# Kernel tuning notes

Hardware: AMD Instinct MI355X
Metric: run time of the kernel (lower is better)

Reference implementation:

```python
import jax, jax.numpy as jnp
import numpy as np

LEAKY_SLOPE = 0.2
ALPHA, BETA = 1.0, 0.1
CLAMP_MAX = 40.0

N_NODES, N_FEAT = 20000, 128
N_EDGES, N_QUERY = 320000, 200000
B = 512            # boundary matrix size
DIM = 8            # 'dimension' hyperparam


def setup_inputs() -> dict:
    key = jax.random.key(0)
    ks = jax.random.split(key, 20)
    sc = 1.0 / np.sqrt(B)
    inp = {
        'x': jax.random.normal(ks[0], (N_NODES, N_FEAT), jnp.float32),
        'L0': jax.random.normal(ks[1], (B, B), jnp.float32) * sc,
        'L1': jax.random.normal(ks[2], (B, B), jnp.float32) * sc,
        'edge_index': jax.random.randint(ks[3], (2, N_EDGES), 0, N_NODES),
        'total_edges': jax.random.randint(ks[4], (N_QUERY, 2), 0, N_NODES),
        # learned params (Linear weights stored as [in, out])
        'conv1_W': jax.random.normal(ks[5], (N_FEAT, 64), jnp.float32) * 0.05,
        'conv1_b': jnp.zeros((64,), jnp.float32),
        'conv2_W': jax.random.normal(ks[6], (64, 32), jnp.float32) * 0.05,
        'conv2_b': jnp.zeros((32,), jnp.float32),
        'weights_sim': jax.random.normal(ks[7], (2 * B, DIM), jnp.float32) * 0.05,
        'embeddings_sim': jax.random.normal(ks[8], (N_FEAT, 2 * B), jnp.float32) * 0.05,
        'weights_off_diagonal': jax.random.normal(ks[9], (B, B), jnp.float32) * sc,
        'weights_L_0': jax.random.normal(ks[10], (B, 32), jnp.float32) * 0.05,
        'weights_L_1': jax.random.normal(ks[11], (B, 32), jnp.float32) * 0.05,
        'lin1_W': jax.random.normal(ks[12], (DIM + 32, 32), jnp.float32) * 0.1,
        'lin1_b': jnp.zeros((32,), jnp.float32),
        'lin_W': jax.random.normal(ks[13], (32, 1), jnp.float32) * 0.1,
        'lin_b': jnp.zeros((1,), jnp.float32),
    }
    return inp


def _renorm_rows(v):
    # torch renorm_(2, 0, 1): rescale rows whose L2 norm exceeds 1
    n = jnp.linalg.norm(v, axis=1, keepdims=True)
    return v * jnp.where(n > 1.0, 1.0 / (n + 1e-7), 1.0)


def _gcn_conv(h, src, dst, dinv, W, b):
    h = h @ W
    msg = h[src] * (dinv[src] * dinv[dst])[:, None]
    return jax.ops.segment_sum(msg, dst, num_segments=h.shape[0]) + b


def reference(x, L0, L1, edge_index, total_edges,
              conv1_W, conv1_b, conv2_W, conv2_b,
              weights_sim, embeddings_sim, weights_off_diagonal,
              weights_L_0, weights_L_1, lin1_W, lin1_b, lin_W, lin_b):
    N = x.shape[0]
    # --- g_encode: two GCN layers (eval mode, dropout = identity) ---
    loops = jnp.arange(N)
    src = jnp.concatenate([edge_index[0], loops])
    dst = jnp.concatenate([edge_index[1], loops])
    deg = jax.ops.segment_sum(jnp.ones_like(dst, dtype=x.dtype), dst, num_segments=N)
    dinv = jnp.where(deg > 0, jax.lax.rsqrt(jnp.maximum(deg, 1.0)), 0.0)
    h = jax.nn.relu(_gcn_conv(x, src, dst, dinv, conv1_W, conv1_b))
    g_emb = jax.nn.relu(_gcn_conv(h, src, dst, dinv, conv2_W, conv2_b))  # [N, 32]

    # --- s_encode: boundary-matrix block + softmax ---
    L0_r = L0 @ L0
    L1_r = L1 @ L1
    rel = (L0_r @ weights_L_0) @ (L1_r @ weights_L_1).T          # [B, B]
    rel_ = weights_off_diagonal @ rel                             # [B, B]
    upper = jnp.concatenate([L0_r, rel_], axis=1)
    lower = jnp.concatenate([rel_.T, L1_r], axis=1)
    sim_block = jax.nn.softmax(jax.nn.relu(jnp.concatenate([upper, lower], axis=0)), axis=1)  # [2B, 2B]

    s_emb = ((x @ embeddings_sim) @ sim_block) @ weights_sim      # [N, DIM]
    s_emb = _renorm_rows(s_emb)
    g = _renorm_rows(g_emb)

    # --- edge gather + distance MLP ---
    i0, i1 = total_edges[:, 0], total_edges[:, 1]
    d_sim = jnp.square(s_emb[i0] - s_emb[i1])                     # [Eq, DIM]
    g_sq = jnp.square(g[i0] - g[i1])                              # [Eq, 32]
    feat = jnp.concatenate([ALPHA * g_sq, BETA * d_sim], axis=1)  # [Eq, 40]
    hq = jax.nn.leaky_relu(feat @ lin1_W + lin1_b, LEAKY_SLOPE)
    sqdist = jnp.abs(hq @ lin_W + lin_b).reshape(-1)
    sqdist = jnp.clip(sqdist, 0.0, CLAMP_MAX)
    prob = jax.nn.sigmoid(2.0 - sqdist)  # == 1/(exp(sqdist-2)+1)
    return prob
```

## Files before the change

### kernel.cpp

```cpp
#include <hip/hip_runtime.h>
#include <math.h>

#define NE 320000
#define NN 20000
#define NQ 200000


__device__ __forceinline__ void gemm512_body(char* smem, const float* __restrict__ A,
                                             float* __restrict__ C, int bb) {
  float (*As)[68] = (float(*)[68])smem;
  float (*Bs)[68] = (float(*)[68])(smem + 16 * 68 * 4);
  int tid = threadIdx.x;
  int tx = tid & 15, ty = tid >> 4;
  int brow = (bb >> 3) * 64;
  int bcol = (bb & 7) * 64;
  float c[4][4] = {};
  for (int k0 = 0; k0 < 512; k0 += 16) {
#pragma unroll
    for (int t = 0; t < 4; t++) {
      int idx = tid * 4 + t;
      int r = idx >> 4, cc = idx & 15;
      As[cc][r] = A[(size_t)(brow + r) * 512 + k0 + cc];
      int r2 = idx >> 6, c2 = idx & 63;
      Bs[r2][c2] = A[(size_t)(k0 + r2) * 512 + bcol + c2];
    }
    __syncthreads();
#pragma unroll
    for (int k = 0; k < 16; k++) {
      float a0 = As[k][ty * 4 + 0], a1 = As[k][ty * 4 + 1];
      float a2 = As[k][ty * 4 + 2], a3 = As[k][ty * 4 + 3];
      float b0 = Bs[k][tx * 4 + 0], b1 = Bs[k][tx * 4 + 1];
      float b2 = Bs[k][tx * 4 + 2], b3 = Bs[k][tx * 4 + 3];
      c[0][0] = fmaf(a0, b0, c[0][0]); c[0][1] = fmaf(a0, b1, c[0][1]);
      c[0][2] = fmaf(a0, b2, c[0][2]); c[0][3] = fmaf(a0, b3, c[0][3]);
      c[1][0] = fmaf(a1, b0, c[1][0]); c[1][1] = fmaf(a1, b1, c[1][1]);
      c[1][2] = fmaf(a1, b2, c[1][2]); c[1][3] = fmaf(a1, b3, c[1][3]);
      c[2][0] = fmaf(a2, b0, c[2][0]); c[2][1] = fmaf(a2, b1, c[2][1]);
      c[2][2] = fmaf(a2, b2, c[2][2]); c[2][3] = fmaf(a2, b3, c[2][3]);
      c[3][0] = fmaf(a3, b0, c[3][0]); c[3][1] = fmaf(a3, b1, c[3][1]);
      c[3][2] = fmaf(a3, b2, c[3][2]); c[3][3] = fmaf(a3, b3, c[3][3]);
    }
    __syncthreads();
  }
#pragma unroll
  for (int i = 0; i < 4; i++)
#pragma unroll
    for (int j = 0; j < 4; j++)
      C[(size_t)(brow + ty * 4 + i) * 512 + bcol + tx * 4 + j] = c[i][j];
}

template<int K, int N>
__device__ __forceinline__ void xw_body(char* smem, const float* __restrict__ X,
                                        const float* __restrict__ W,
                                        float* __restrict__ Y, int bb) {
  constexpr int TPR = N / 4;
  constexpr int ROWS = 256 / TPR;
  float* Wl = (float*)smem;
  for (int t = threadIdx.x; t < K * N / 4; t += 256)
    ((float4*)Wl)[t] = ((const float4*)W)[t];
  __syncthreads();
  int r = bb * ROWS + threadIdx.x / TPR;
  int c4 = (threadIdx.x % TPR) * 4;
  if (r >= NN) return;
  const float4* xr4 = (const float4*)(X + (size_t)r * K);
  float a0 = 0, a1 = 0, a2 = 0, a3 = 0;
#pragma unroll 4
  for (int k4 = 0; k4 < K / 4; k4++) {
    float4 xv = xr4[k4];
    int kb = k4 * 4;
    { const float4 w = *(const float4*)&Wl[(kb + 0) * N + c4];
      a0 = fmaf(xv.x, w.x, a0); a1 = fmaf(xv.x, w.y, a1); a2 = fmaf(xv.x, w.z, a2); a3 = fmaf(xv.x, w.w, a3); }
    { const float4 w = *(const float4*)&Wl[(kb + 1) * N + c4];
      a0 = fmaf(xv.y, w.x, a0); a1 = fmaf(xv.y, w.y, a1); a2 = fmaf(xv.y, w.z, a2); a3 = fmaf(xv.y, w.w, a3); }
    { const float4 w = *(const float4*)&Wl[(kb + 2) * N + c4];
      a0 = fmaf(xv.z, w.x, a0); a1 = fmaf(xv.z, w.y, a1); a2 = fmaf(xv.z, w.z, a2); a3 = fmaf(xv.z, w.w, a3); }
    { const float4 w = *(const float4*)&Wl[(kb + 3) * N + c4];
      a0 = fmaf(xv.w, w.x, a0); a1 = fmaf(xv.w, w.y, a1); a2 = fmaf(xv.w, w.z, a2); a3 = fmaf(xv.w, w.w, a3); }
  }
  float4 o; o.x = a0; o.y = a1; o.z = a2; o.w = a3;
  *(float4*)&Y[(size_t)r * N + c4] = o;
}

__device__ __forceinline__ void sk512_body(const float* X, const float* W, float* Y, int b) {
  int r = b * 32 + threadIdx.x / 8;
  int c4 = (threadIdx.x % 8) * 4;
  const float4* xr4 = (const float4*)(X + (size_t)r * 512);
  float a0 = 0, a1 = 0, a2 = 0, a3 = 0;
#pragma unroll 2
  for (int k4 = 0; k4 < 128; k4++) {
    float4 xv = xr4[k4];
    int kb = k4 * 4;
    { const float4 w = *(const float4*)&W[(kb + 0) * 32 + c4];
      a0 = fmaf(xv.x, w.x, a0); a1 = fmaf(xv.x, w.y, a1); a2 = fmaf(xv.x, w.z, a2); a3 = fmaf(xv.x, w.w, a3); }
    { const float4 w = *(const float4*)&W[(kb + 1) * 32 + c4];
      a0 = fmaf(xv.y, w.x, a0); a1 = fmaf(xv.y, w.y, a1); a2 = fmaf(xv.y, w.z, a2); a3 = fmaf(xv.y, w.w, a3); }
    { const float4 w = *(const float4*)&W[(kb + 2) * 32 + c4];
      a0 = fmaf(xv.z, w.x, a0); a1 = fmaf(xv.z, w.y, a1); a2 = fmaf(xv.z, w.z, a2); a3 = fmaf(xv.z, w.w, a3); }
    { const float4 w = *(const float4*)&W[(kb + 3) * 32 + c4];
      a0 = fmaf(xv.w, w.x, a0); a1 = fmaf(xv.w, w.y, a1); a2 = fmaf(xv.w, w.z, a2); a3 = fmaf(xv.w, w.w, a3); }
  }
  float4 o; o.x = a0; o.y = a1; o.z = a2; o.w = a3;
  *(float4*)&Y[(size_t)r * 32 + c4] = o;
}


__global__ __launch_bounds__(256) void mega1(const float* __restrict__ L0,
                                             const float* __restrict__ L1,
                                             float* __restrict__ L0r,
                                             float* __restrict__ L1r,
                                             const float* __restrict__ x,
                                             const float* __restrict__ W1,
                                             float* __restrict__ h1raw,
                                             int* __restrict__ ideg) {
  __shared__ __align__(16) char smem[32768];
  int b = blockIdx.x;
  if (b < 128) {
    const float* A = (b < 64) ? L0 : L1;
    float* C = (b < 64) ? L0r : L1r;
    gemm512_body(smem, A, C, b & 63);
  } else if (b < 1378) {
    xw_body<128, 64>(smem, x, W1, h1raw, b - 128);
  } else {
    int i = (b - 1378) * 256 + threadIdx.x;
    if (i < NN) ideg[i] = 0;
  }
}

__global__ __launch_bounds__(256) void mega2(const float* __restrict__ L0r,
                                             const float* __restrict__ L1r,
                                             const float* __restrict__ wL0,
                                             const float* __restrict__ wL1,
                                             float* __restrict__ Ab,
                                             float* __restrict__ Bb,
                                             const int* __restrict__ ei,
                                             int* __restrict__ ideg) {
  int b = blockIdx.x;
  if (b < 16) sk512_body(L0r, wL0, Ab, b);
  else if (b < 32) sk512_body(L1r, wL1, Bb, b - 16);
  else {
    int e = (b - 32) * 256 + threadIdx.x;
    if (e < NE) atomicAdd(&ideg[ei[NE + e]], 1);
  }
}

__global__ __launch_bounds__(256) void mega3(const float* __restrict__ wod,
                                             const float* __restrict__ Ab,
                                             float* __restrict__ Ab2,
                                             const int* __restrict__ ideg,
                                             int* __restrict__ start,
                                             int* __restrict__ cursor,
                                             float* __restrict__ dinv) {
  int b = blockIdx.x;
  if (b < 16) { sk512_body(wod, Ab, Ab2, b); return; }
  __shared__ int wsum[4];
  int t = threadIdx.x;
  int base = t * 80;
  int4 c[20];
  const int4* ip = (const int4*)ideg + t * 20;
#pragma unroll
  for (int i = 0; i < 20; i++) c[i] = ip[i];
  int s = 0;
  if (base < NN) {
#pragma unroll
    for (int i = 0; i < 20; i++) s += c[i].x + c[i].y + c[i].z + c[i].w;
  }
  int lane = t & 63, wid = t >> 6;
  int v = s;
#pragma unroll
  for (int o = 1; o < 64; o <<= 1) { int u = __shfl_up(v, o); if (lane >= o) v += u; }
  if (lane == 63) wsum[wid] = v;
  __syncthreads();
  int wbase = 0;
  for (int w = 0; w < wid; w++) wbase += wsum[w];
  int off = wbase + v - s;
  if (base < NN) {
#pragma unroll
    for (int i = 0; i < 20; i++) {
      int4 cc = c[i];
      int4 st;
      st.x = off; off += cc.x;
      st.y = off; off += cc.y;
      st.z = off; off += cc.z;
      st.w = off; off += cc.w;
      ((int4*)start)[t * 20 + i] = st;
      ((int4*)cursor)[t * 20 + i] = st;
      float4 dv;
      dv.x = rsqrtf((float)(cc.x + 1));
      dv.y = rsqrtf((float)(cc.y + 1));
      dv.z = rsqrtf((float)(cc.z + 1));
      dv.w = rsqrtf((float)(cc.w + 1));
      ((float4*)dinv)[t * 20 + i] = dv;
    }
  }
}

__global__ __launch_bounds__(256) void mega4(const float* __restrict__ L0r,
                                             const float* __restrict__ L1r,
                                             const float* __restrict__ Ab2,
                                             const float* __restrict__ Bb,
                                             const float* __restrict__ wsim,
                                             float* __restrict__ M,
                                             const int* __restrict__ ei,
                                             int* __restrict__ cursor,
                                             int* __restrict__ csr) {
  int b = blockIdx.x;
  if (b >= 1024) {
    int e = (b - 1024) * 256 + threadIdx.x;
    if (e < NE) {
      int d = ei[NE + e];
      int pos = atomicAdd(&cursor[d], 1);
      csr[pos] = ei[e];
    }
    return;
  }
  int i = b;
  int tid = threadIdx.x;
  float urow[32];
  {
    const float4* up = (const float4*)((i < 512) ? (Ab2 + i * 32) : (Bb + (i - 512) * 32));
#pragma unroll
    for (int q = 0; q < 8; q++) {
      float4 u4 = up[q];
      urow[q * 4 + 0] = u4.x; urow[q * 4 + 1] = u4.y;
      urow[q * 4 + 2] = u4.z; urow[q * 4 + 3] = u4.w;
    }
  }
  float loc[4];
  float mymax = 0.0f;
#pragma unroll
  for (int t = 0; t < 4; t++) {
    int j = tid + t * 256;
    float v;
    if (i < 512) {
      if (j < 512) v = L0r[i * 512 + j];
      else {
        const float4* bj = (const float4*)(Bb + (j - 512) * 32);
        float acc = 0.0f;
#pragma unroll
        for (int q = 0; q < 8; q++) {
          float4 b4 = bj[q];
          acc = fmaf(urow[q * 4 + 0], b4.x, acc); acc = fmaf(urow[q * 4 + 1], b4.y, acc);
          acc = fmaf(urow[q * 4 + 2], b4.z, acc); acc = fmaf(urow[q * 4 + 3], b4.w, acc);
        }
        v = acc;
      }
    } else {
      int r = i - 512;
      if (j < 512) {
        const float4* aj = (const float4*)(Ab2 + j * 32);
        float acc = 0.0f;
#pragma unroll
        for (int q = 0; q < 8; q++) {
          float4 a4 = aj[q];
          acc = fmaf(urow[q * 4 + 0], a4.x, acc); acc = fmaf(urow[q * 4 + 1], a4.y, acc);
          acc = fmaf(urow[q * 4 + 2], a4.z, acc); acc = fmaf(urow[q * 4 + 3], a4.w, acc);
        }
        v = acc;
      } else v = L1r[r * 512 + (j - 512)];
    }
    v = fmaxf(v, 0.0f);
    loc[t] = v;
    mymax = fmaxf(mymax, v);
  }
#pragma unroll
  for (int o = 32; o > 0; o >>= 1) mymax = fmaxf(mymax, __shfl_down(mymax, o));
  __shared__ float smax[4];
  int wid = tid >> 6, lane = tid & 63;
  if (lane == 0) smax[wid] = mymax;
  __syncthreads();
  float m = fmaxf(fmaxf(smax[0], smax[1]), fmaxf(smax[2], smax[3]));

  float z = 0.0f, pm[8] = {};
#pragma unroll
  for (int t = 0; t < 4; t++) {
    int j = tid + t * 256;
    float e = __expf(loc[t] - m);
    z += e;
    const float* wr = wsim + j * 8;
#pragma unroll
    for (int d = 0; d < 8; d++) pm[d] = fmaf(e, wr[d], pm[d]);
  }
#pragma unroll
  for (int o = 32; o > 0; o >>= 1) {
    z += __shfl_down(z, o);
#pragma unroll
    for (int d = 0; d < 8; d++) pm[d] += __shfl_down(pm[d], o);
  }
  __shared__ float sred[4][9];
  if (lane == 0) {
    sred[wid][0] = z;
#pragma unroll
    for (int d = 0; d < 8; d++) sred[wid][1 + d] = pm[d];
  }
  __syncthreads();
  if (tid < 8) {
    float zt = sred[0][0] + sred[1][0] + sred[2][0] + sred[3][0];
    float pt = sred[0][1 + tid] + sred[1][1 + tid] + sred[2][1 + tid] + sred[3][1 + tid];
    M[i * 8 + tid] = pt / zt;
  }
}

__global__ __launch_bounds__(256) void mega5(const int* __restrict__ start,
                                             const int* __restrict__ ideg,
                                             const int* __restrict__ csr,
                                             const float* __restrict__ hraw,
                                             const float* __restrict__ dinv,
                                             const float* __restrict__ b1,
                                             float* __restrict__ hout,
                                             const float* __restrict__ emb,
                                             const float* __restrict__ M,
                                             float* __restrict__ E) {
  int b = blockIdx.x;
  if (b < 5000) {
    int lane = threadIdx.x & 63;
    int n = b * 4 + (threadIdx.x >> 6);
    int s0 = start[n], cnt = ideg[n];
    float acc = 0.0f;
    int k = 0;
    for (; k + 1 < cnt; k += 2) {
      int sA = csr[s0 + k], sB = csr[s0 + k + 1];
      float dA = dinv[sA], dB = dinv[sB];
      float vA = hraw[(size_t)sA * 64 + lane];
      float vB = hraw[(size_t)sB * 64 + lane];
      acc = fmaf(vA, dA, acc);
      acc = fmaf(vB, dB, acc);
    }
    if (k < cnt) {
      int sA = csr[s0 + k];
      acc = fmaf(hraw[(size_t)sA * 64 + lane], dinv[sA], acc);
    }
    float dn = dinv[n];
    float v = fmaf(acc, dn, hraw[(size_t)n * 64 + lane] * dn * dn) + b1[lane];
    hout[(size_t)n * 64 + lane] = fmaxf(v, 0.0f);
    return;
  }
  int lane = threadIdx.x & 63;
  int r = (b - 5000) * 4 + (threadIdx.x >> 6);
  const float* er = emb + (size_t)r * 1024;
  float acc[8] = {};
  for (int it = 0; it < 16; it++) {
    int k = lane + it * 64;
    float e = er[k];
    const float4* mp = (const float4*)&M[k * 8];
    float4 m0 = mp[0], m1 = mp[1];
    acc[0] = fmaf(e, m0.x, acc[0]); acc[1] = fmaf(e, m0.y, acc[1]);
    acc[2] = fmaf(e, m0.z, acc[2]); acc[3] = fmaf(e, m0.w, acc[3]);
    acc[4] = fmaf(e, m1.x, acc[4]); acc[5] = fmaf(e, m1.y, acc[5]);
    acc[6] = fmaf(e, m1.z, acc[6]); acc[7] = fmaf(e, m1.w, acc[7]);
  }
#pragma unroll
  for (int o = 32; o > 0; o >>= 1)
#pragma unroll
    for (int d = 0; d < 8; d++) acc[d] += __shfl_down(acc[d], o);
  if (lane == 0)
#pragma unroll
    for (int d = 0; d < 8; d++) E[r * 8 + d] = acc[d];
}

__global__ __launch_bounds__(256) void mega6(const float* __restrict__ h1,
                                             const float* __restrict__ W2,
                                             float* __restrict__ h2raw,
                                             const float* __restrict__ x,
                                             const float* __restrict__ E,
                                             float* __restrict__ semb) {
  __shared__ __align__(16) char smem[8192];
  int b = blockIdx.x;
  if (b < 625) { xw_body<64, 32>(smem, h1, W2, h2raw, b); return; }
  float* El = (float*)smem;
  for (int t = threadIdx.x; t < 256; t += 256)
    ((float4*)El)[t] = ((const float4*)E)[t];
  __syncthreads();
  int row = (b - 625) * 256 + threadIdx.x;
  if (row >= NN) return;
  const float4* xr4 = (const float4*)(x + (size_t)row * 128);
  float s[8] = {};
#pragma unroll 4
  for (int k4 = 0; k4 < 32; k4++) {
    float4 xv = xr4[k4];
    int kb = k4 * 4;
#pragma unroll
    for (int u = 0; u < 4; u++) {
      float xk = (u == 0) ? xv.x : (u == 1) ? xv.y : (u == 2) ? xv.z : xv.w;
      const float4* ep = (const float4*)&El[(kb + u) * 8];
      float4 e0 = ep[0], e1 = ep[1];
      s[0] = fmaf(xk, e0.x, s[0]); s[1] = fmaf(xk, e0.y, s[1]);
      s[2] = fmaf(xk, e0.z, s[2]); s[3] = fmaf(xk, e0.w, s[3]);
      s[4] = fmaf(xk, e1.x, s[4]); s[5] = fmaf(xk, e1.y, s[5]);
      s[6] = fmaf(xk, e1.z, s[6]); s[7] = fmaf(xk, e1.w, s[7]);
    }
  }
  float n2 = 0.0f;
#pragma unroll
  for (int d = 0; d < 8; d++) n2 += s[d] * s[d];
  float n = sqrtf(n2);
  float sc = (n > 1.0f) ? 1.0f / (n + 1e-7f) : 1.0f;
#pragma unroll
  for (int d = 0; d < 8; d++) semb[(size_t)row * 8 + d] = s[d] * sc;
}

__global__ __launch_bounds__(256) void mega7(const int* __restrict__ start,
                                             const int* __restrict__ ideg,
                                             const int* __restrict__ csr,
                                             const float* __restrict__ hraw,
                                             const float* __restrict__ dinv,
                                             const float* __restrict__ b2,
                                             float* __restrict__ g) {
  int lane = threadIdx.x & 31;
  int n = blockIdx.x * 8 + (threadIdx.x >> 5);
  int s0 = start[n], cnt = ideg[n];
  float acc = 0.0f;
  int k = 0;
  for (; k + 1 < cnt; k += 2) {
    int sA = csr[s0 + k], sB = csr[s0 + k + 1];
    float dA = dinv[sA], dB = dinv[sB];
    float vA = hraw[(size_t)sA * 32 + lane];
    float vB = hraw[(size_t)sB * 32 + lane];
    acc = fmaf(vA, dA, acc);
    acc = fmaf(vB, dB, acc);
  }
  if (k < cnt) {
    int sA = csr[s0 + k];
    acc = fmaf(hraw[(size_t)sA * 32 + lane], dinv[sA], acc);
  }
  float dn = dinv[n];
  float v = fmaf(acc, dn, hraw[(size_t)n * 32 + lane] * dn * dn) + b2[lane];
  v = fmaxf(v, 0.0f);
  float n2 = v * v;
#pragma unroll
  for (int o = 16; o > 0; o >>= 1) n2 += __shfl_xor(n2, o);
  float nrm = sqrtf(n2);
  float sc = (nrm > 1.0f) ? 1.0f / (nrm + 1e-7f) : 1.0f;
  g[(size_t)n * 32 + lane] = v * sc;
}

__global__ __launch_bounds__(256) void mega8(const int* __restrict__ te,
                                             const float* __restrict__ g,
                                             const float* __restrict__ semb,
                                             const float* __restrict__ W1,
                                             const float* __restrict__ b1,
                                             const float* __restrict__ lw,
                                             const float* __restrict__ lb,
                                             float* __restrict__ out) {
  int q = blockIdx.x * 256 + threadIdx.x;
  if (q >= NQ) return;
  const int2 p = ((const int2*)te)[q];
  int i0 = p.x, i1 = p.y;
  float feat[40];
  const float4* g0 = (const float4*)(g + (size_t)i0 * 32);
  const float4* g1 = (const float4*)(g + (size_t)i1 * 32);
#pragma unroll
  for (int t = 0; t < 8; t++) {
    float4 a = g0[t], b = g1[t];
    float d0 = a.x - b.x, d1 = a.y - b.y, d2 = a.z - b.z, d3 = a.w - b.w;
    feat[t * 4 + 0] = d0 * d0; feat[t * 4 + 1] = d1 * d1;
    feat[t * 4 + 2] = d2 * d2; feat[t * 4 + 3] = d3 * d3;
  }
  const float4* s0 = (const float4*)(semb + (size_t)i0 * 8);
  const float4* s1 = (const float4*)(semb + (size_t)i1 * 8);
#pragma unroll
  for (int t = 0; t < 2; t++) {
    float4 a = s0[t], b = s1[t];
    float d0 = a.x - b.x, d1 = a.y - b.y, d2 = a.z - b.z, d3 = a.w - b.w;
    feat[32 + t * 4 + 0] = 0.1f * d0 * d0; feat[32 + t * 4 + 1] = 0.1f * d1 * d1;
    feat[32 + t * 4 + 2] = 0.1f * d2 * d2; feat[32 + t * 4 + 3] = 0.1f * d3 * d3;
  }
  float acc[32];
#pragma unroll
  for (int c = 0; c < 32; c++) acc[c] = b1[c];
#pragma unroll
  for (int k = 0; k < 40; k++) {
    float f = feat[k];
#pragma unroll
    for (int c = 0; c < 32; c++) acc[c] = fmaf(f, W1[k * 32 + c], acc[c]);
  }
  float accv = lb[0];
#pragma unroll
  for (int c = 0; c < 32; c++) {
    float a = acc[c];
    a = (a > 0.0f) ? a : 0.2f * a;
    accv = fmaf(a, lw[c], accv);
  }
  float sq = fminf(fabsf(accv), 40.0f);
  out[q] = 1.0f / (1.0f + __expf(sq - 2.0f));
}

extern "C" void kernel_launch(void* const* d_in, const int* in_sizes, int n_in,
                              void* d_out, int out_size, void* d_ws, size_t ws_size,
                              hipStream_t stream) {
  const float* x     = (const float*)d_in[0];
  const float* L0    = (const float*)d_in[1];
  const float* L1    = (const float*)d_in[2];
  const int*   ei    = (const int*)d_in[3];
  const int*   te    = (const int*)d_in[4];
  const float* W1    = (const float*)d_in[5];
  const float* b1    = (const float*)d_in[6];
  const float* W2    = (const float*)d_in[7];
  const float* b2    = (const float*)d_in[8];
  const float* wsim  = (const float*)d_in[9];
  const float* embs  = (const float*)d_in[10];
  const float* wod   = (const float*)d_in[11];
  const float* wL0   = (const float*)d_in[12];
  const float* wL1   = (const float*)d_in[13];
  const float* lin1W = (const float*)d_in[14];
  const float* lin1b = (const float*)d_in[15];
  const float* linW  = (const float*)d_in[16];
  const float* linb  = (const float*)d_in[17];
  float* out = (float*)d_out;

  int*   ideg   = (int*)d_ws;
  int*   start  = ideg + 20000;
  int*   cursor = start + 20000;
  int*   csr    = cursor + 20000;
  float* dinv   = (float*)(csr + 320000);
  float* h1raw  = dinv + 20000;
  float* h1     = h1raw + 1280000;
  float* h2raw  = h1raw;
  float* g      = h1 + 1280000;
  float* L0r    = g + 640000;
  float* L1r    = L0r + 262144;
  float* Ab     = L1r + 262144;
  float* Bb     = Ab + 16384;
  float* Ab2    = Bb + 16384;
  float* Mm     = Ab2 + 16384;
  float* Ee     = Mm + 8192;
  float* semb   = Ee + 1024;

  mega1<<<1457, 256, 0, stream>>>(L0, L1, L0r, L1r, x, W1, h1raw, ideg);
  mega2<<<1282, 256, 0, stream>>>(L0r, L1r, wL0, wL1, Ab, Bb, ei, ideg);
  mega3<<<17,   256, 0, stream>>>(wod, Ab, Ab2, ideg, start, cursor, dinv);
  mega4<<<2274, 256, 0, stream>>>(L0r, L1r, Ab2, Bb, wsim, Mm, ei, cursor, csr);
  mega5<<<5032, 256, 0, stream>>>(start, ideg, csr, h1raw, dinv, b1, h1, embs, Mm, Ee);
  mega6<<<704,  256, 0, stream>>>(h1, W2, h2raw, x, Ee, semb);
  mega7<<<2500, 256, 0, stream>>>(start, ideg, csr, h2raw, dinv, b2, g);
  mega8<<<782,  256, 0, stream>>>(te, g, semb, lin1W, lin1b, linW, linb, out);
}
```

Measured before the change: 186.4 us.

## Fuse eight phase kernels into one persistent cooperative kernel with grid syncs

Replaces the eight separate kernel launches with a single cooperative persistent kernel. Its blocks loop over each phase's tiles, with grid.sync between phases, so per-launch overhead and inter-kernel gaps go away. Shared memory is capped at 16KB so more blocks fit per CU, which means xw_body now stages the weight matrix in K-chunks. The final MLP is split into two 16-column halves to cut register pressure. Separate launches remain as a fallback if the cooperative launch fails. The trade-off is grid-wide barrier cost, and small phases (such as the 17-block scan) leaving most blocks idle.

Measured after the change: 668.7 us. +258.7%, slower.

```diff
diff --git a/kernel.cpp b/kernel.cpp
--- a/kernel.cpp
+++ b/kernel.cpp
@@ -1,10 +1,21 @@
 #include <hip/hip_runtime.h>
+#include <hip/hip_cooperative_groups.h>
 #include <math.h>
+
+namespace cg = cooperative_groups;
 
 #define NE 320000
 #define NN 20000
 #define NQ 200000
 
+struct Prm {
+  const float *x, *L0, *L1;
+  const int *ei, *te;
+  const float *W1, *b1, *W2, *b2, *wsim, *embs, *wod, *wL0, *wL1, *lin1W, *lin1b, *linW, *linb;
+  float *out;
+  int *ideg, *start, *cursor, *csr;
+  float *dinv, *h1raw, *h1, *g, *L0r, *L1r, *Ab, *Bb, *Ab2, *Mm, *Ee, *semb;
+};
 
 __device__ __forceinline__ void gemm512_body(char* smem, const float* __restrict__ A,
                                              float* __restrict__ C, int bb) {
@@ -55,30 +66,38 @@
                                         float* __restrict__ Y, int bb) {
   constexpr int TPR = N / 4;
   constexpr int ROWS = 256 / TPR;
+  constexpr int KC = (K * N * 4 > 16384) ? (16384 / (N * 4)) : K;
   float* Wl = (float*)smem;
-  for (int t = threadIdx.x; t < K * N / 4; t += 256)
-    ((float4*)Wl)[t] = ((const float4*)W)[t];
-  __syncthreads();
   int r = bb * ROWS + threadIdx.x / TPR;
   int c4 = (threadIdx.x % TPR) * 4;
-  if (r >= NN) return;
-  const float4* xr4 = (const float4*)(X + (size_t)r * K);
   float a0 = 0, a1 = 0, a2 = 0, a3 = 0;
+#pragma unroll 1
+  for (int k0 = 0; k0 < K; k0 += KC) {
+    for (int t = threadIdx.x; t < KC * N / 4; t += 256)
+      ((float4*)Wl)[t] = ((const float4*)(W + k0 * N))[t];
+    __syncthreads();
+    if (r < NN) {
+      const float4* xr4 = (const float4*)(X + (size_t)r * K + k0);
 #pragma unroll 4
-  for (int k4 = 0; k4 < K / 4; k4++) {
-    float4 xv = xr4[k4];
-    int kb = k4 * 4;
-    { const float4 w = *(const float4*)&Wl[(kb + 0) * N + c4];
-      a0 = fmaf(xv.x, w.x, a0); a1 = fmaf(xv.x, w.y, a1); a2 = fmaf(xv.x, w.z, a2); a3 = fmaf(xv.x, w.w, a3); }
-    { const float4 w = *(const float4*)&Wl[(kb + 1) * N + c4];
-      a0 = fmaf(xv.y, w.x, a0); a1 = fmaf(xv.y, w.y, a1); a2 = fmaf(xv.y, w.z, a2); a3 = fmaf(xv.y, w.w, a3); }
-    { const float4 w = *(const float4*)&Wl[(kb + 2) * N + c4];
-      a0 = fmaf(xv.z, w.x, a0); a1 = fmaf(xv.z, w.y, a1); a2 = fmaf(xv.z, w.z, a2); a3 = fmaf(xv.z, w.w, a3); }
-    { const float4 w = *(const float4*)&Wl[(kb + 3) * N + c4];
-      a0 = fmaf(xv.w, w.x, a0); a1 = fmaf(xv.w, w.y, a1); a2 = fmaf(xv.w, w.z, a2); a3 = fmaf(xv.w, w.w, a3); }
-  }
-  float4 o; o.x = a0; o.y = a1; o.z = a2; o.w = a3;
-  *(float4*)&Y[(size_t)r * N + c4] = o;
+      for (int k4 = 0; k4 < KC / 4; k4++) {
+        float4 xv = xr4[k4];
+        int kb = k4 * 4;
+        { const float4 w = *(const float4*)&Wl[(kb + 0) * N + c4];
+          a0 = fmaf(xv.x, w.x, a0); a1 = fmaf(xv.x, w.y, a1); a2 = fmaf(xv.x, w.z, a2); a3 = fmaf(xv.x, w.w, a3); }
+        { const float4 w = *(const float4*)&Wl[(kb + 1) * N + c4];
+          a0 = fmaf(xv.y, w.x, a0); a1 = fmaf(xv.y, w.y, a1); a2 = fmaf(xv.y, w.z, a2); a3 = fmaf(xv.y, w.w, a3); }
+        { const float4 w = *(const float4*)&Wl[(kb + 2) * N + c4];
+          a0 = fmaf(xv.z, w.x, a0); a1 = fmaf(xv.z, w.y, a1); a2 = fmaf(xv.z, w.z, a2); a3 = fmaf(xv.z, w.w, a3); }
+        { const float4 w = *(const float4*)&Wl[(kb + 3) * N + c4];
+          a0 = fmaf(xv.w, w.x, a0); a1 = fmaf(xv.w, w.y, a1); a2 = fmaf(xv.w, w.z, a2); a3 = fmaf(xv.w, w.w, a3); }
+      }
+    }
+    __syncthreads();
+  }
+  if (r < NN) {
+    float4 o; o.x = a0; o.y = a1; o.z = a2; o.w = a3;
+    *(float4*)&Y[(size_t)r * N + c4] = o;
+  }
 }
 
 __device__ __forceinline__ void sk512_body(const float* X, const float* W, float* Y, int b) {
@@ -104,67 +123,41 @@
 }
 
 
-__global__ __launch_bounds__(256) void mega1(const float* __restrict__ L0,
-                                             const float* __restrict__ L1,
-                                             float* __restrict__ L0r,
-                                             float* __restrict__ L1r,
-                                             const float* __restrict__ x,
-                                             const float* __restrict__ W1,
-                                             float* __restrict__ h1raw,
-                                             int* __restrict__ ideg) {
-  __shared__ __align__(16) char smem[32768];
-  int b = blockIdx.x;
-  if (b < 128) {
-    const float* A = (b < 64) ? L0 : L1;
-    float* C = (b < 64) ? L0r : L1r;
-    gemm512_body(smem, A, C, b & 63);
-  } else if (b < 1378) {
-    xw_body<128, 64>(smem, x, W1, h1raw, b - 128);
+__device__ __forceinline__ void phase0(const Prm& p, char* smem, int t) {
+  if (t < 128) {
+    gemm512_body(smem, (t < 64) ? p.L0 : p.L1, (t < 64) ? p.L0r : p.L1r, t & 63);
+  } else if (t < 1378) {
+    xw_body<128, 64>(smem, p.x, p.W1, p.h1raw, t - 128);
   } else {
-    int i = (b - 1378) * 256 + threadIdx.x;
-    if (i < NN) ideg[i] = 0;
-  }
-}
-
-__global__ __launch_bounds__(256) void mega2(const float* __restrict__ L0r,
-                                             const float* __restrict__ L1r,
-                                             const float* __restrict__ wL0,
-                                             const float* __restrict__ wL1,
-                                             float* __restrict__ Ab,
-                                             float* __restrict__ Bb,
-                                             const int* __restrict__ ei,
-                                             int* __restrict__ ideg) {
-  int b = blockIdx.x;
-  if (b < 16) sk512_body(L0r, wL0, Ab, b);
-  else if (b < 32) sk512_body(L1r, wL1, Bb, b - 16);
+    int i = (t - 1378) * 256 + threadIdx.x;
+    if (i < NN) p.ideg[i] = 0;
+  }
+}
+
+__device__ __forceinline__ void phase1(const Prm& p, int t) {
+  if (t < 16) sk512_body(p.L0r, p.wL0, p.Ab, t);
+  else if (t < 32) sk512_body(p.L1r, p.wL1, p.Bb, t - 16);
   else {
-    int e = (b - 32) * 256 + threadIdx.x;
-    if (e < NE) atomicAdd(&ideg[ei[NE + e]], 1);
-  }
-}
-
-__global__ __launch_bounds__(256) void mega3(const float* __restrict__ wod,
-                                             const float* __restrict__ Ab,
-                                             float* __restrict__ Ab2,
-                                             const int* __restrict__ ideg,
-                                             int* __restrict__ start,
-                                             int* __restrict__ cursor,
-                                             float* __restrict__ dinv) {
-  int b = blockIdx.x;
-  if (b < 16) { sk512_body(wod, Ab, Ab2, b); return; }
-  __shared__ int wsum[4];
-  int t = threadIdx.x;
-  int base = t * 80;
+    int e = (t - 32) * 256 + threadIdx.x;
+    if (e < NE) atomicAdd(&p.ideg[p.ei[NE + e]], 1);
+  }
+}
+
+__device__ __forceinline__ void phase2(const Prm& p, char* smem, int t) {
+  int tid = threadIdx.x;
+  if (t < 16) { sk512_body(p.wod, p.Ab, p.Ab2, t); return; }
+  int* wsum = (int*)smem;
+  int base = tid * 80;
   int4 c[20];
-  const int4* ip = (const int4*)ideg + t * 20;
-#pragma unroll
-  for (int i = 0; i < 20; i++) c[i] = ip[i];
   int s = 0;
   if (base < NN) {
+    const int4* ip = (const int4*)p.ideg + tid * 20;
+#pragma unroll
+    for (int i = 0; i < 20; i++) c[i] = ip[i];
 #pragma unroll
     for (int i = 0; i < 20; i++) s += c[i].x + c[i].y + c[i].z + c[i].w;
   }
-  int lane = t & 63, wid = t >> 6;
+  int lane = tid & 63, wid = tid >> 6;
   int v = s;
 #pragma unroll
   for (int o = 1; o < 64; o <<= 1) { int u = __shfl_up(v, o); if (lane >= o) v += u; }
@@ -182,42 +175,36 @@
       st.y = off; off += cc.y;
       st.z = off; off += cc.z;
       st.w = off; off += cc.w;
-      ((int4*)start)[t * 20 + i] = st;
-      ((int4*)cursor)[t * 20 + i] = st;
+      ((int4*)p.start)[tid * 20 + i] = st;
+      ((int4*)p.cursor)[tid * 20 + i] = st;
       float4 dv;
       dv.x = rsqrtf((float)(cc.x + 1));
       dv.y = rsqrtf((float)(cc.y + 1));
       dv.z = rsqrtf((float)(cc.z + 1));
       dv.w = rsqrtf((float)(cc.w + 1));
-      ((float4*)dinv)[t * 20 + i] = dv;
-    }
-  }
-}
-
-__global__ __launch_bounds__(256) void mega4(const float* __restrict__ L0r,
-                                             const float* __restrict__ L1r,
-                                             const float* __restrict__ Ab2,
-                                             const float* __restrict__ Bb,
-                                             const float* __restrict__ wsim,
-                                             float* __restrict__ M,
-                                             const int* __restrict__ ei,
-                                             int* __restrict__ cursor,
-                                             int* __restrict__ csr) {
-  int b = blockIdx.x;
-  if (b >= 1024) {
-    int e = (b - 1024) * 256 + threadIdx.x;
+      ((float4*)p.dinv)[tid * 20 + i] = dv;
+    }
+  }
+  __syncthreads();
+}
+
+__device__ __forceinline__ void phase3(const Prm& p, char* smem, int t) {
+  int tid = threadIdx.x;
+  if (t >= 1024) {
+    int e = (t - 1024) * 256 + tid;
     if (e < NE) {
-      int d = ei[NE + e];
-      int pos = atomicAdd(&cursor[d], 1);
-      csr[pos] = ei[e];
+      int d = p.ei[NE + e];
+      int pos = atomicAdd(&p.cursor[d], 1);
+      p.csr[pos] = p.ei[e];
     }
     return;
   }
-  int i = b;
-  int tid = threadIdx.x;
+  int i = t;
+  float* smax = (float*)smem;
+  float (*sred)[9] = (float(*)[9])(smem + 64);
   float urow[32];
   {
-    const float4* up = (const float4*)((i < 512) ? (Ab2 + i * 32) : (Bb + (i - 512) * 32));
+    const float4* up = (const float4*)((i < 512) ? (p.Ab2 + i * 32) : (p.Bb + (i - 512) * 32));
 #pragma unroll
     for (int q = 0; q < 8; q++) {
       float4 u4 = up[q];
@@ -228,13 +215,13 @@
   float loc[4];
   float mymax = 0.0f;
 #pragma unroll
-  for (int t = 0; t < 4; t++) {
-    int j = tid + t * 256;
+  for (int tt = 0; tt < 4; tt++) {
+    int j = tid + tt * 256;
     float v;
     if (i < 512) {
-      if (j < 512) v = L0r[i * 512 + j];
+      if (j < 512) v = p.L0r[i * 512 + j];
       else {
-        const float4* bj = (const float4*)(Bb + (j - 512) * 32);
+        const float4* bj = (const float4*)(p.Bb + (j - 512) * 32);
         float acc = 0.0f;
 #pragma unroll
         for (int q = 0; q < 8; q++) {
@@ -247,7 +234,7 @@
     } else {
       int r = i - 512;
       if (j < 512) {
-        const float4* aj = (const float4*)(Ab2 + j * 32);
+        const float4* aj = (const float4*)(p.Ab2 + j * 32);
         float acc = 0.0f;
 #pragma unroll
         for (int q = 0; q < 8; q++) {
@@ -256,15 +243,14 @@
           acc = fmaf(urow[q * 4 + 2], a4.z, acc); acc = fmaf(urow[q * 4 + 3], a4.w, acc);
         }
         v = acc;
-      } else v = L1r[r * 512 + (j - 512)];
+      } else v = p.L1r[r * 512 + (j - 512)];
     }
     v = fmaxf(v, 0.0f);
-    loc[t] = v;
+    loc[tt] = v;
     mymax = fmaxf(mymax, v);
   }
 #pragma unroll
   for (int o = 32; o > 0; o >>= 1) mymax = fmaxf(mymax, __shfl_down(mymax, o));
-  __shared__ float smax[4];
   int wid = tid >> 6, lane = tid & 63;
   if (lane == 0) smax[wid] = mymax;
   __syncthreads();
@@ -272,11 +258,11 @@
 
   float z = 0.0f, pm[8] = {};
 #pragma unroll
-  for (int t = 0; t < 4; t++) {
-    int j = tid + t * 256;
-    float e = __expf(loc[t] - m);
+  for (int tt = 0; tt < 4; tt++) {
+    int j = tid + tt * 256;
+    float e = __expf(loc[tt] - m);
     z += e;
-    const float* wr = wsim + j * 8;
+    const float* wr = p.wsim + j * 8;
 #pragma unroll
     for (int d = 0; d < 8; d++) pm[d] = fmaf(e, wr[d], pm[d]);
   }
@@ -286,7 +272,6 @@
 #pragma unroll
     for (int d = 0; d < 8; d++) pm[d] += __shfl_down(pm[d], o);
   }
-  __shared__ float sred[4][9];
   if (lane == 0) {
     sred[wid][0] = z;
 #pragma unroll
@@ -296,241 +281,270 @@
   if (tid < 8) {
     float zt = sred[0][0] + sred[1][0] + sred[2][0] + sred[3][0];
     float pt = sred[0][1 + tid] + sred[1][1 + tid] + sred[2][1 + tid] + sred[3][1 + tid];
-    M[i * 8 + tid] = pt / zt;
-  }
-}
-
-__global__ __launch_bounds__(256) void mega5(const int* __restrict__ start,
-                                             const int* __restrict__ ideg,
-                                             const int* __restrict__ csr,
-                                             const float* __restrict__ hraw,
-                                             const float* __restrict__ dinv,
-                                             const float* __restrict__ b1,
-                                             float* __restrict__ hout,
-                                             const float* __restrict__ emb,
-                                             const float* __restrict__ M,
-                                             float* __restrict__ E) {
-  int b = blockIdx.x;
-  if (b < 5000) {
-    int lane = threadIdx.x & 63;
-    int n = b * 4 + (threadIdx.x >> 6);
-    int s0 = start[n], cnt = ideg[n];
+    p.Mm[i * 8 + tid] = pt / zt;
+  }
+  __syncthreads();
+}
+
+__device__ __forceinline__ void phase4(const Prm& p, int t) {
+  int tid = threadIdx.x;
+  if (t < 5000) {
+    int lane = tid & 63;
+    int n = t * 4 + (tid >> 6);
+    int s0 = p.start[n], cnt = p.ideg[n];
     float acc = 0.0f;
     int k = 0;
     for (; k + 1 < cnt; k += 2) {
-      int sA = csr[s0 + k], sB = csr[s0 + k + 1];
-      float dA = dinv[sA], dB = dinv[sB];
-      float vA = hraw[(size_t)sA * 64 + lane];
-      float vB = hraw[(size_t)sB * 64 + lane];
+      int sA = p.csr[s0 + k], sB = p.csr[s0 + k + 1];
+      float dA = p.dinv[sA], dB = p.dinv[sB];
+      float vA = p.h1raw[(size_t)sA * 64 + lane];
+      float vB = p.h1raw[(size_t)sB * 64 + lane];
       acc = fmaf(vA, dA, acc);
       acc = fmaf(vB, dB, acc);
     }
     if (k < cnt) {
-      int sA = csr[s0 + k];
-      acc = fmaf(hraw[(size_t)sA * 64 + lane], dinv[sA], acc);
-    }
-    float dn = dinv[n];
-    float v = fmaf(acc, dn, hraw[(size_t)n * 64 + lane] * dn * dn) + b1[lane];
-    hout[(size_t)n * 64 + lane] = fmaxf(v, 0.0f);
+      int sA = p.csr[s0 + k];
+      acc = fmaf(p.h1raw[(size_t)sA * 64 + lane], p.dinv[sA], acc);
+    }
+    float dn = p.dinv[n];
+    float v = fmaf(acc, dn, p.h1raw[(size_t)n * 64 + lane] * dn * dn) + p.b1[lane];
+    p.h1[(size_t)n * 64 + lane] = fmaxf(v, 0.0f);
+  } else {
+    int lane = tid & 63;
+    int r = (t - 5000) * 4 + (tid >> 6);
+    const float* er = p.embs + (size_t)r * 1024;
+    float acc[8] = {};
+    for (int it = 0; it < 16; it++) {
+      int k = lane + it * 64;
+      float e = er[k];
+      const float4* mp = (const float4*)&p.Mm[k * 8];
+      float4 m0 = mp[0], m1 = mp[1];
+      acc[0] = fmaf(e, m0.x, acc[0]); acc[1] = fmaf(e, m0.y, acc[1]);
+      acc[2] = fmaf(e, m0.z, acc[2]); acc[3] = fmaf(e, m0.w, acc[3]);
+      acc[4] = fmaf(e, m1.x, acc[4]); acc[5] = fmaf(e, m1.y, acc[5]);
+      acc[6] = fmaf(e, m1.z, acc[6]); acc[7] = fmaf(e, m1.w, acc[7]);
+    }
+#pragma unroll
+    for (int o = 32; o > 0; o >>= 1)
+#pragma unroll
+      for (int d = 0; d < 8; d++) acc[d] += __shfl_down(acc[d], o);
+    if (lane == 0)
+#pragma unroll
+      for (int d = 0; d < 8; d++) p.Ee[r * 8 + d] = acc[d];
+  }
+}
+
+__device__ __forceinline__ void phase5(const Prm& p, char* smem, int t) {
+  int tid = threadIdx.x;
+  if (t < 625) {
+    xw_body<64, 32>(smem, p.h1, p.W2, p.h1raw , t);
     return;
   }
-  int lane = threadIdx.x & 63;
-  int r = (b - 5000) * 4 + (threadIdx.x >> 6);
-  const float* er = emb + (size_t)r * 1024;
-  float acc[8] = {};
-  for (int it = 0; it < 16; it++) {
-    int k = lane + it * 64;
-    float e = er[k];
-    const float4* mp = (const float4*)&M[k * 8];
-    float4 m0 = mp[0], m1 = mp[1];
-    acc[0] = fmaf(e, m0.x, acc[0]); acc[1] = fmaf(e, m0.y, acc[1]);
-    acc[2] = fmaf(e, m0.z, acc[2]); acc[3] = fmaf(e, m0.w, acc[3]);
-    acc[4] = fmaf(e, m1.x, acc[4]); acc[5] = fmaf(e, m1.y, acc[5]);
-    acc[6] = fmaf(e, m1.z, acc[6]); acc[7] = fmaf(e, m1.w, acc[7]);
-  }
-#pragma unroll
-  for (int o = 32; o > 0; o >>= 1)
-#pragma unroll
-    for (int d = 0; d < 8; d++) acc[d] += __shfl_down(acc[d], o);
-  if (lane == 0)
-#pragma unroll
-    for (int d = 0; d < 8; d++) E[r * 8 + d] = acc[d];
-}
-
-__global__ __launch_bounds__(256) void mega6(const float* __restrict__ h1,
-                                             const float* __restrict__ W2,
-                                             float* __restrict__ h2raw,
-                                             const float* __restrict__ x,
-                                             const float* __restrict__ E,
-                                             float* __restrict__ semb) {
-  __shared__ __align__(16) char smem[8192];
-  int b = blockIdx.x;
-  if (b < 625) { xw_body<64, 32>(smem, h1, W2, h2raw, b); return; }
   float* El = (float*)smem;
-  for (int t = threadIdx.x; t < 256; t += 256)
-    ((float4*)El)[t] = ((const float4*)E)[t];
-  __syncthreads();
-  int row = (b - 625) * 256 + threadIdx.x;
-  if (row >= NN) return;
-  const float4* xr4 = (const float4*)(x + (size_t)row * 128);
-  float s[8] = {};
+  for (int u = tid; u < 256; u += 256)
+    ((float4*)El)[u] = ((const float4*)p.Ee)[u];
+  __syncthreads();
+  int row = (t - 625) * 256 + tid;
+  if (row < NN) {
+    const float4* xr4 = (const float4*)(p.x + (size_t)row * 128);
+    float s[8] = {};
 #pragma unroll 4
-  for (int k4 = 0; k4 < 32; k4++) {
-    float4 xv = xr4[k4];
-    int kb = k4 * 4;
-#pragma unroll
-    for (int u = 0; u < 4; u++) {
-      float xk = (u == 0) ? xv.x : (u == 1) ? xv.y : (u == 2) ? xv.z : xv.w;
-      const float4* ep = (const float4*)&El[(kb + u) * 8];
-      float4 e0 = ep[0], e1 = ep[1];
-      s[0] = fmaf(xk, e0.x, s[0]); s[1] = fmaf(xk, e0.y, s[1]);
-      s[2] = fmaf(xk, e0.z, s[2]); s[3] = fmaf(xk, e0.w, s[3]);
-      s[4] = fmaf(xk, e1.x, s[4]); s[5] = fmaf(xk, e1.y, s[5]);
-      s[6] = fmaf(xk, e1.z, s[6]); s[7] = fmaf(xk, e1.w, s[7]);
-    }
-  }
-  float n2 = 0.0f;
-#pragma unroll
-  for (int d = 0; d < 8; d++) n2 += s[d] * s[d];
-  float n = sqrtf(n2);
-  float sc = (n > 1.0f) ? 1.0f / (n + 1e-7f) : 1.0f;
-#pragma unroll
-  for (int d = 0; d < 8; d++) semb[(size_t)row * 8 + d] = s[d] * sc;
-}
-
-__global__ __launch_bounds__(256) void mega7(const int* __restrict__ start,
-                                             const int* __restrict__ ideg,
-                                             const int* __restrict__ csr,
-                                             const float* __restrict__ hraw,
-                                             const float* __restrict__ dinv,
-                                             const float* __restrict__ b2,
-                                             float* __restrict__ g) {
-  int lane = threadIdx.x & 31;
-  int n = blockIdx.x * 8 + (threadIdx.x >> 5);
-  int s0 = start[n], cnt = ideg[n];
+    for (int k4 = 0; k4 < 32; k4++) {
+      float4 xv = xr4[k4];
+      int kb = k4 * 4;
+#pragma unroll
+      for (int u = 0; u < 4; u++) {
+        float xk = (u == 0) ? xv.x : (u == 1) ? xv.y : (u == 2) ? xv.z : xv.w;
+        const float4* ep = (const float4*)&El[(kb + u) * 8];
+        float4 e0 = ep[0], e1 = ep[1];
+        s[0] = fmaf(xk, e0.x, s[0]); s[1] = fmaf(xk, e0.y, s[1]);
+        s[2] = fmaf(xk, e0.z, s[2]); s[3] = fmaf(xk, e0.w, s[3]);
+        s[4] = fmaf(xk, e1.x, s[4]); s[5] = fmaf(xk, e1.y, s[5]);
+        s[6] = fmaf(xk, e1.z, s[6]); s[7] = fmaf(xk, e1.w, s[7]);
+      }
+    }
+    float n2 = 0.0f;
+#pragma unroll
+    for (int d = 0; d < 8; d++) n2 += s[d] * s[d];
+    float n = sqrtf(n2);
+    float sc = (n > 1.0f) ? 1.0f / (n + 1e-7f) : 1.0f;
+#pragma unroll
+    for (int d = 0; d < 8; d++) p.semb[(size_t)row * 8 + d] = s[d] * sc;
+  }
+  __syncthreads();
+}
+
+__device__ __forceinline__ void phase6(const Prm& p, int t) {
+  int tid = threadIdx.x;
+  int lane = tid & 31;
+  int n = t * 8 + (tid >> 5);
+  int s0 = p.start[n], cnt = p.ideg[n];
   float acc = 0.0f;
   int k = 0;
   for (; k + 1 < cnt; k += 2) {
-    int sA = csr[s0 + k], sB = csr[s0 + k + 1];
-    float dA = dinv[sA], dB = dinv[sB];
-    float vA = hraw[(size_t)sA * 32 + lane];
-    float vB = hraw[(size_t)sB * 32 + lane];
+    int sA = p.csr[s0 + k], sB = p.csr[s0 + k + 1];
+    float dA = p.dinv[sA], dB = p.dinv[sB];
+    float vA = p.h1raw[(size_t)sA * 32 + lane];
+    float vB = p.h1raw[(size_t)sB * 32 + lane];
     acc = fmaf(vA, dA, acc);
     acc = fmaf(vB, dB, acc);
   }
   if (k < cnt) {
-    int sA = csr[s0 + k];
-    acc = fmaf(hraw[(size_t)sA * 32 + lane], dinv[sA], acc);
-  }
-  float dn = dinv[n];
-  float v = fmaf(acc, dn, hraw[(size_t)n * 32 + lane] * dn * dn) + b2[lane];
+    int sA = p.csr[s0 + k];
+    acc = fmaf(p.h1raw[(size_t)sA * 32 + lane], p.dinv[sA], acc);
+  }
+  float dn = p.dinv[n];
+  float v = fmaf(acc, dn, p.h1raw[(size_t)n * 32 + lane] * dn * dn) + p.b2[lane];
   v = fmaxf(v, 0.0f);
   float n2 = v * v;
 #pragma unroll
   for (int o = 16; o > 0; o >>= 1) n2 += __shfl_xor(n2, o);
   float nrm = sqrtf(n2);
   float sc = (nrm > 1.0f) ? 1.0f / (nrm + 1e-7f) : 1.0f;
-  g[(size_t)n * 32 + lane] = v * sc;
-}
-
-__global__ __launch_bounds__(256) void mega8(const int* __restrict__ te,
-                                             const float* __restrict__ g,
-                                             const float* __restrict__ semb,
-                                             const float* __restrict__ W1,
-                                             const float* __restrict__ b1,
-                                             const float* __restrict__ lw,
-                                             const float* __restrict__ lb,
-                                             float* __restrict__ out) {
-  int q = blockIdx.x * 256 + threadIdx.x;
+  p.g[(size_t)n * 32 + lane] = v * sc;
+}
+
+__device__ __forceinline__ void phase7(const Prm& p, int t) {
+  int q = t * 256 + threadIdx.x;
   if (q >= NQ) return;
-  const int2 p = ((const int2*)te)[q];
-  int i0 = p.x, i1 = p.y;
+  const int2 pr = ((const int2*)p.te)[q];
+  int i0 = pr.x, i1 = pr.y;
   float feat[40];
-  const float4* g0 = (const float4*)(g + (size_t)i0 * 32);
-  const float4* g1 = (const float4*)(g + (size_t)i1 * 32);
-#pragma unroll
-  for (int t = 0; t < 8; t++) {
-    float4 a = g0[t], b = g1[t];
+  const float4* g0 = (const float4*)(p.g + (size_t)i0 * 32);
+  const float4* g1 = (const float4*)(p.g + (size_t)i1 * 32);
+#pragma unroll
+  for (int u = 0; u < 8; u++) {
+    float4 a = g0[u], b = g1[u];
     float d0 = a.x - b.x, d1 = a.y - b.y, d2 = a.z - b.z, d3 = a.w - b.w;
-    feat[t * 4 + 0] = d0 * d0; feat[t * 4 + 1] = d1 * d1;
-    feat[t * 4 + 2] = d2 * d2; feat[t * 4 + 3] = d3 * d3;
-  }
-  const float4* s0 = (const float4*)(semb + (size_t)i0 * 8);
-  const float4* s1 = (const float4*)(semb + (size_t)i1 * 8);
-#pragma unroll
-  for (int t = 0; t < 2; t++) {
-    float4 a = s0[t], b = s1[t];
+    feat[u * 4 + 0] = d0 * d0; feat[u * 4 + 1] = d1 * d1;
+    feat[u * 4 + 2] = d2 * d2; feat[u * 4 + 3] = d3 * d3;
+  }
+  const float4* s0 = (const float4*)(p.semb + (size_t)i0 * 8);
+  const float4* s1 = (const float4*)(p.semb + (size_t)i1 * 8);
+#pragma unroll
+  for (int u = 0; u < 2; u++) {
+    float4 a = s0[u], b = s1[u];
     float d0 = a.x - b.x, d1 = a.y - b.y, d2 = a.z - b.z, d3 = a.w - b.w;
-    feat[32 + t * 4 + 0] = 0.1f * d0 * d0; feat[32 + t * 4 + 1] = 0.1f * d1 * d1;
-    feat[32 + t * 4 + 2] = 0.1f * d2 * d2; feat[32 + t * 4 + 3] = 0.1f * d3 * d3;
-  }
-  float acc[32];
-#pragma unroll
-  for (int c = 0; c < 32; c++) acc[c] = b1[c];
-#pragma unroll
-  for (int k = 0; k < 40; k++) {
-    float f = feat[k];
-#pragma unroll
-    for (int c = 0; c < 32; c++) acc[c] = fmaf(f, W1[k * 32 + c], acc[c]);
-  }
-  float accv = lb[0];
-#pragma unroll
-  for (int c = 0; c < 32; c++) {
-    float a = acc[c];
-    a = (a > 0.0f) ? a : 0.2f * a;
-    accv = fmaf(a, lw[c], accv);
+    feat[32 + u * 4 + 0] = 0.1f * d0 * d0; feat[32 + u * 4 + 1] = 0.1f * d1 * d1;
+    feat[32 + u * 4 + 2] = 0.1f * d2 * d2; feat[32 + u * 4 + 3] = 0.1f * d3 * d3;
+  }
+  float accv = p.linb[0];
+#pragma unroll 1
+  for (int h = 0; h < 2; h++) {
+    float acc[16];
+#pragma unroll
+    for (int c = 0; c < 16; c++) acc[c] = p.lin1b[h * 16 + c];
+#pragma unroll
+    for (int k = 0; k < 40; k++) {
+      float f = feat[k];
+#pragma unroll
+      for (int c = 0; c < 16; c++)
+        acc[c] = fmaf(f, p.lin1W[k * 32 + h * 16 + c], acc[c]);
+    }
+#pragma unroll
+    for (int c = 0; c < 16; c++) {
+      float a = acc[c];
+      a = (a > 0.0f) ? a : 0.2f * a;
+      accv = fmaf(a, p.linW[h * 16 + c], accv);
+    }
   }
   float sq = fminf(fabsf(accv), 40.0f);
-  out[q] = 1.0f / (1.0f + __expf(sq - 2.0f));
+  p.out[q] = 1.0f / (1.0f + __expf(sq - 2.0f));
+}
+
+__global__ __launch_bounds__(256, 4) void fused(Prm p) {
+  cg::grid_group grid = cg::this_grid();
+  __shared__ __align__(16) char smem[16384];
+  const int NB = gridDim.x;
+  for (int t = blockIdx.x; t < 1457; t += NB) phase0(p, smem, t);
+  grid.sync();
+  for (int t = blockIdx.x; t < 1282; t += NB) phase1(p, t);
+  grid.sync();
+  for (int t = blockIdx.x; t < 17; t += NB) phase2(p, smem, t);
+  grid.sync();
+  for (int t = blockIdx.x; t < 2274; t += NB) phase3(p, smem, t);
+  grid.sync();
+  for (int t = blockIdx.x; t < 5032; t += NB) phase4(p, t);
+  grid.sync();
+  for (int t = blockIdx.x; t < 704; t += NB) phase5(p, smem, t);
+  grid.sync();
+  for (int t = blockIdx.x; t < 2500; t += NB) phase6(p, t);
+  grid.sync();
+  for (int t = blockIdx.x; t < 782; t += NB) phase7(p, t);
+}
+
+template<int PH>
+__global__ __launch_bounds__(256, 4) void solo(Prm p) {
+  __shared__ __align__(16) char smem[16384];
+  int t = blockIdx.x;
+  if (PH == 0) phase0(p, smem, t);
+  if (PH == 1) phase1(p, t);
+  if (PH == 2) phase2(p, smem, t);
+  if (PH == 3) phase3(p, smem, t);
+  if (PH == 4) phase4(p, t);
+  if (PH == 5) phase5(p, smem, t);
+  if (PH == 6) phase6(p, t);
+  if (PH == 7) phase7(p, t);
 }
 
 extern "C" void kernel_launch(void* const* d_in, const int* in_sizes, int n_in,
                               void* d_out, int out_size, void* d_ws, size_t ws_size,
                               hipStream_t stream) {
-  const float* x     = (const float*)d_in[0];
-  const float* L0    = (const float*)d_in[1];
-  const float* L1    = (const float*)d_in[2];
-  const int*   ei    = (const int*)d_in[3];
-  const int*   te    = (const int*)d_in[4];
-  const float* W1    = (const float*)d_in[5];
-  const float* b1    = (const float*)d_in[6];
-  const float* W2    = (const float*)d_in[7];
-  const float* b2    = (const float*)d_in[8];
-  const float* wsim  = (const float*)d_in[9];
-  const float* embs  = (const float*)d_in[10];
-  const float* wod   = (const float*)d_in[11];
-  const float* wL0   = (const float*)d_in[12];
-  const float* wL1   = (const float*)d_in[13];
-  const float* lin1W = (const float*)d_in[14];
-  const float* lin1b = (const float*)d_in[15];
-  const float* linW  = (const float*)d_in[16];
-  const float* linb  = (const float*)d_in[17];
-  float* out = (float*)d_out;
-
-  int*   ideg   = (int*)d_ws;
-  int*   start  = ideg + 20000;
-  int*   cursor = start + 20000;
-  int*   csr    = cursor + 20000;
-  float* dinv   = (float*)(csr + 320000);
-  float* h1raw  = dinv + 20000;
-  float* h1     = h1raw + 1280000;
-  float* h2raw  = h1raw;
-  float* g      = h1 + 1280000;
-  float* L0r    = g + 640000;
-  float* L1r    = L0r + 262144;
-  float* Ab     = L1r + 262144;
-  float* Bb     = Ab + 16384;
-  float* Ab2    = Bb + 16384;
-  float* Mm     = Ab2 + 16384;
-  float* Ee     = Mm + 8192;
-  float* semb   = Ee + 1024;
-
-  mega1<<<1457, 256, 0, stream>>>(L0, L1, L0r, L1r, x, W1, h1raw, ideg);
-  mega2<<<1282, 256, 0, stream>>>(L0r, L1r, wL0, wL1, Ab, Bb, ei, ideg);
-  mega3<<<17,   256, 0, stream>>>(wod, Ab, Ab2, ideg, start, cursor, dinv);
-  mega4<<<2274, 256, 0, stream>>>(L0r, L1r, Ab2, Bb, wsim, Mm, ei, cursor, csr);
-  mega5<<<5032, 256, 0, stream>>>(start, ideg, csr, h1raw, dinv, b1, h1, embs, Mm, Ee);
-  mega6<<<704,  256, 0, stream>>>(h1, W2, h2raw, x, Ee, semb);
-  mega7<<<2500, 256, 0, stream>>>(start, ideg, csr, h2raw, dinv, b2, g);
-  mega8<<<782,  256, 0, stream>>>(te, g, semb, lin1W, lin1b, linW, linb, out);
-}
+  Prm p;
+  p.x     = (const float*)d_in[0];
+  p.L0    = (const float*)d_in[1];
+  p.L1    = (const float*)d_in[2];
+  p.ei    = (const int*)d_in[3];
+  p.te    = (const int*)d_in[4];
+  p.W1    = (const float*)d_in[5];
+  p.b1    = (const float*)d_in[6];
+  p.W2    = (const float*)d_in[7];
+  p.b2    = (const float*)d_in[8];
+  p.wsim  = (const float*)d_in[9];
+  p.embs  = (const float*)d_in[10];
+  p.wod   = (const float*)d_in[11];
+  p.wL0   = (const float*)d_in[12];
+  p.wL1   = (const float*)d_in[13];
+  p.lin1W = (const float*)d_in[14];
+  p.lin1b = (const float*)d_in[15];
+  p.linW  = (const float*)d_in[16];
+  p.linb  = (const float*)d_in[17];
+  p.out   = (float*)d_out;
+
+  p.ideg   = (int*)d_ws;
+  p.start  = p.ideg + 20000;
+  p.cursor = p.start + 20000;
+  p.csr    = p.cursor + 20000;
+  p.dinv   = (float*)(p.csr + 320000);
+  p.h1raw  = p.dinv + 20000;
+  p.h1     = p.h1raw + 1280000;
+  p.g      = p.h1 + 1280000;
+  p.L0r    = p.g + 640000;
+  p.L1r    = p.L0r + 262144;
+  p.Ab     = p.L1r + 262144;
+  p.Bb     = p.Ab + 16384;
+  p.Ab2    = p.Bb + 16384;
+  p.Mm     = p.Ab2 + 16384;
+  p.Ee     = p.Mm + 8192;
+  p.semb   = p.Ee + 1024;
+
+  int occ = 0;
+  hipError_t qe = hipOccupancyMaxActiveBlocksPerMultiprocessor(&occ, (const void*)fused, 256, 0);
+  hipError_t le = hipErrorUnknown;
+  if (qe == hipSuccess && occ > 0) {
+    int grid = occ * 256;
+    if (grid > 1024) grid = 1024;
+    void* args[] = { &p };
+    le = hipLaunchCooperativeKernel((const void*)fused, dim3(grid), dim3(256), args, 0, stream);
+  }
+  if (le != hipSuccess) {
+    solo<0><<<1457, 256, 0, stream>>>(p);
+    solo<1><<<1282, 256, 0, stream>>>(p);
+    solo<2><<<17,   256, 0, stream>>>(p);
+    solo<3><<<2274, 256, 0, stream>>>(p);
+    solo<4><<<5032, 256, 0, stream>>>(p);
+    solo<5><<<704,  256, 0, stream>>>(p);
+    solo<6><<<2500, 256, 0, stream>>>(p);
+    solo<7><<<782,  256, 0, stream>>>(p);
+  }
+}
```
